# Kernel tuning notes

Hardware: AMD Instinct MI355X
Metric: run time of the kernel (lower is better)

Reference implementation:

```python
import jax, jax.numpy as jnp
import numpy as np

B, T, LATENT, FFN, TEMB = 4, 4096, 256, 1024, 2048
D = 8 * LATENT  # 2048
LN_EPS = 1e-5


def setup_inputs() -> dict:
    key = jax.random.key(0)
    ks = jax.random.split(key, 12)
    s1 = 1.0 / np.sqrt(LATENT)
    s2 = 1.0 / np.sqrt(FFN)
    sd = 1.0 / np.sqrt(D)
    st = 1.0 / np.sqrt(TEMB)
    return {
        "x": jax.random.normal(ks[0], (B, T, D), dtype=jnp.float32),
        "emb": jax.random.normal(ks[1], (B, TEMB), dtype=jnp.float32),
        # 8 parallel branch weights, batched along leading expert axis
        "W1": jax.random.uniform(ks[2], (8, LATENT, FFN), jnp.float32, -s1, s1),
        "b1": jax.random.uniform(ks[3], (8, FFN), jnp.float32, -s1, s1),
        "W2": jax.random.uniform(ks[4], (8, FFN, LATENT), jnp.float32, -s2, s2),
        "b2": jax.random.uniform(ks[5], (8, LATENT), jnp.float32, -s2, s2),
        # StylizationBlock params (latent_dim*8 = D)
        "emb_W": jax.random.uniform(ks[6], (TEMB, 2 * D), jnp.float32, -st, st),
        "emb_b": jax.random.uniform(ks[7], (2 * D,), jnp.float32, -st, st),
        "ln_g": jnp.ones((D,), jnp.float32),
        "ln_b": jnp.zeros((D,), jnp.float32),
        "out_W": jax.random.uniform(ks[8], (D, D), jnp.float32, -sd, sd),
        "out_b": jax.random.uniform(ks[9], (D,), jnp.float32, -sd, sd),
    }


def _layernorm(h, g, b):
    mu = jnp.mean(h, axis=-1, keepdims=True)
    var = jnp.mean(jnp.square(h - mu), axis=-1, keepdims=True)
    return (h - mu) * jax.lax.rsqrt(var + LN_EPS) * g + b


def reference(x, emb, W1, b1, W2, b2, emb_W, emb_b, ln_g, ln_b, out_W, out_b):
    Bx, Tx, Dx = x.shape
    xr = x.reshape(Bx, Tx, 8, LATENT)  # (B,T,8,latent)
    # 8 parallel Linear->GELU->Linear chains as batched GEMMs
    h = jnp.einsum("btel,elf->btef", xr, W1) + b1  # (B,T,8,ffn)
    h = jax.nn.gelu(h, approximate=False)  # dropout=0 (eval)
    y = jnp.einsum("btef,efl->btel", h, W2) + b2  # (B,T,8,latent)
    y = y.reshape(Bx, Tx, Dx)  # concat along channels
    # StylizationBlock: scale/shift from time emb, LN, SiLU, Linear
    eo = jax.nn.silu(emb) @ emb_W + emb_b  # (B, 2D)
    scale, shift = jnp.split(eo[:, None, :], 2, axis=-1)  # (B,1,D) each
    hn = _layernorm(y, ln_g, ln_b) * (1.0 + scale) + shift
    proj = jax.nn.silu(hn) @ out_W + out_b  # (B,T,D)
    return x + proj
```

## Files before the change

### kernel.cpp

```cpp
#include <hip/hip_runtime.h>

typedef __attribute__((ext_vector_type(8))) __bf16 bf16x8;
typedef __attribute__((ext_vector_type(4))) __bf16 bf16x4;
typedef __attribute__((ext_vector_type(4))) float f32x4;

#define TOKENS 16384
#define DDIM   2048
#define LAT    256
#define FFND   1024

__global__ void transpose_f32_bf16(const float* __restrict__ src, __bf16* __restrict__ dst,
                                   int R, int C) {
  __shared__ float tile[32][33];
  const int b = blockIdx.z;
  src += (size_t)b * R * C;
  dst += (size_t)b * R * C;
  const int c0 = blockIdx.x * 32, r0 = blockIdx.y * 32;
  const int tx = threadIdx.x & 31, ty = threadIdx.x >> 5;
  for (int i = ty; i < 32; i += 8)
    tile[i][tx] = src[(size_t)(r0 + i) * C + c0 + tx];
  __syncthreads();
  for (int i = ty; i < 32; i += 8)
    dst[(size_t)(c0 + i) * R + r0 + tx] = (__bf16)tile[tx][i];
}

__global__ void k0_partial(const float* __restrict__ emb, const float* __restrict__ embW,
                           float* __restrict__ pp) {
  __shared__ float se[4 * 256];
  const int tid = threadIdx.x;
  const int kc = blockIdx.y;
  const int kb = kc * 256;
  for (int i = tid; i < 1024; i += 256) {
    const int bb = i >> 8, kk = i & 255;
    float v = emb[bb * 2048 + kb + kk];
    se[i] = v / (1.f + __expf(-v));
  }
  __syncthreads();
  const int j = blockIdx.x * 256 + tid;
  float a0 = 0.f, a1 = 0.f, a2 = 0.f, a3 = 0.f;
  for (int k = 0; k < 256; ++k) {
    float wv = embW[(size_t)(kb + k) * 4096 + j];
    a0 += se[k] * wv;
    a1 += se[256 + k] * wv;
    a2 += se[512 + k] * wv;
    a3 += se[768 + k] * wv;
  }
  pp[(size_t)(kc * 4 + 0) * 4096 + j] = a0;
  pp[(size_t)(kc * 4 + 1) * 4096 + j] = a1;
  pp[(size_t)(kc * 4 + 2) * 4096 + j] = a2;
  pp[(size_t)(kc * 4 + 3) * 4096 + j] = a3;
}

__global__ void k0_reduce(const float* __restrict__ pp, const float* __restrict__ embb,
                          float* __restrict__ ss) {
  const int j = blockIdx.x * 256 + threadIdx.x;
  const float bb = embb[j];
#pragma unroll
  for (int b = 0; b < 4; ++b) {
    float s = bb;
#pragma unroll
    for (int kc = 0; kc < 8; ++kc) s += pp[(size_t)(kc * 4 + b) * 4096 + j];
    ss[b * 4096 + j] = s;
  }
}

__launch_bounds__(256, 2)
__global__ void k1_expert_ffn(const float* __restrict__ x, const __bf16* __restrict__ W1T,
                              const float* __restrict__ b1, const __bf16* __restrict__ W2T,
                              const float* __restrict__ b2, __bf16* __restrict__ y) {
  __shared__ __bf16 xs[64 * 256];
  __shared__ __bf16 hs[64 * 256];

  const int tid = threadIdx.x;
  const int w = tid >> 6;
  const int lane = tid & 63;
  const int q = lane >> 4;
  const int ln = lane & 15;
  const int m0 = blockIdx.x * 64;
  const int e = blockIdx.y;

  {
    const int r0 = tid >> 6;
    const int c = (tid & 63) * 4;
#pragma unroll
    for (int p = 0; p < 16; ++p) {
      const int r = r0 + p * 4;
      f32x4 v = *(const f32x4*)(x + (size_t)(m0 + r) * DDIM + e * LAT + c);
      bf16x4 o;
      o[0] = (__bf16)v[0]; o[1] = (__bf16)v[1]; o[2] = (__bf16)v[2]; o[3] = (__bf16)v[3];
      *(bf16x4*)(xs + r * 256 + c) = o;
    }
  }

  f32x4 acc_y[4][4];
#pragma unroll
  for (int j = 0; j < 4; ++j) {
    float bv = b2[e * LAT + w * 64 + j * 16 + ln];
    f32x4 t = {bv, bv, bv, bv};
#pragma unroll
    for (int i = 0; i < 4; ++i) acc_y[i][j] = t;
  }

  __syncthreads();

  for (int fc = 0; fc < 4; ++fc) {
    f32x4 acc_h[4][4];
#pragma unroll
    for (int j = 0; j < 4; ++j) {
      float bv = b1[e * FFND + fc * 256 + w * 64 + j * 16 + ln];
      f32x4 t = {bv, bv, bv, bv};
#pragma unroll
      for (int i = 0; i < 4; ++i) acc_h[i][j] = t;
    }

    const __bf16* w1src = W1T + ((size_t)e * FFND + fc * 256 + w * 64) * LAT;
    for (int k0 = 0; k0 < 256; k0 += 32) {
      bf16x8 af[4], bfr[4];
#pragma unroll
      for (int j = 0; j < 4; ++j)
        bfr[j] = *(const bf16x8*)(w1src + (size_t)(j * 16 + ln) * LAT + k0 + q * 8);
#pragma unroll
      for (int i = 0; i < 4; ++i)
        af[i] = *(const bf16x8*)(xs + (i * 16 + ln) * 256 + k0 + q * 8);
#pragma unroll
      for (int i = 0; i < 4; ++i)
#pragma unroll
        for (int j = 0; j < 4; ++j)
          acc_h[i][j] = __builtin_amdgcn_mfma_f32_16x16x32_bf16(af[i], bfr[j], acc_h[i][j], 0, 0, 0);
    }

    __syncthreads();

#pragma unroll
    for (int i = 0; i < 4; ++i)
#pragma unroll
      for (int j = 0; j < 4; ++j) {
        const int fl = w * 64 + j * 16 + ln;
#pragma unroll
        for (int r = 0; r < 4; ++r) {
          float vv = acc_h[i][j][r];
          float ge = 0.5f * vv * (1.0f + erff(vv * 0.70710678118654752f));
          hs[(i * 16 + q * 4 + r) * 256 + fl] = (__bf16)ge;
        }
      }

    __syncthreads();

    const __bf16* w2src = W2T + ((size_t)e * LAT + w * 64) * FFND + fc * 256;
    for (int k0 = 0; k0 < 256; k0 += 32) {
      bf16x8 af[4], bfr[4];
#pragma unroll
      for (int j = 0; j < 4; ++j)
        bfr[j] = *(const bf16x8*)(w2src + (size_t)(j * 16 + ln) * FFND + k0 + q * 8);
#pragma unroll
      for (int i = 0; i < 4; ++i)
        af[i] = *(const bf16x8*)(hs + (i * 16 + ln) * 256 + k0 + q * 8);
#pragma unroll
      for (int i = 0; i < 4; ++i)
#pragma unroll
        for (int j = 0; j < 4; ++j)
          acc_y[i][j] = __builtin_amdgcn_mfma_f32_16x16x32_bf16(af[i], bfr[j], acc_y[i][j], 0, 0, 0);
    }
  }

#pragma unroll
  for (int i = 0; i < 4; ++i)
#pragma unroll
    for (int j = 0; j < 4; ++j) {
      const int l = w * 64 + j * 16 + ln;
#pragma unroll
      for (int r = 0; r < 4; ++r) {
        const int m = i * 16 + q * 4 + r;
        y[(size_t)(m0 + m) * DDIM + e * LAT + l] = (__bf16)acc_y[i][j][r];
      }
    }
}

__global__ void k2_ln_mod_silu(const float* __restrict__ ss, const float* __restrict__ g,
                               const float* __restrict__ bb, __bf16* __restrict__ y) {
  __shared__ float red[8];
  const int t = blockIdx.x;
  const int b = t >> 12;
  const int tid = threadIdx.x;
  __bf16* row = y + (size_t)t * DDIM;
  bf16x8 v8 = *(bf16x8*)(row + tid * 8);
  float v[8], s = 0.f, sq = 0.f;
#pragma unroll
  for (int i = 0; i < 8; ++i) {
    v[i] = (float)v8[i];
    s += v[i];
    sq += v[i] * v[i];
  }
#pragma unroll
  for (int off = 32; off > 0; off >>= 1) {
    s += __shfl_down(s, off);
    sq += __shfl_down(sq, off);
  }
  if ((tid & 63) == 0) {
    red[tid >> 6] = s;
    red[4 + (tid >> 6)] = sq;
  }
  __syncthreads();
  const float S = red[0] + red[1] + red[2] + red[3];
  const float SQ = red[4] + red[5] + red[6] + red[7];
  const float mean = S * (1.f / DDIM);
  const float var = SQ * (1.f / DDIM) - mean * mean;
  const float rstd = rsqrtf(var + 1e-5f);
  const float* sc = ss + (size_t)b * 2 * DDIM;
#pragma unroll
  for (int i = 0; i < 8; ++i) {
    const int d = tid * 8 + i;
    float hn = (v[i] - mean) * rstd * g[d] + bb[d];
    hn = hn * (1.f + sc[d]) + sc[DDIM + d];
    float si = hn / (1.f + __expf(-hn));
    v8[i] = (__bf16)si;
  }
  *(bf16x8*)(row + tid * 8) = v8;
}

__launch_bounds__(256, 2)
__global__ void k3_proj(const __bf16* __restrict__ a, const __bf16* __restrict__ oWT,
                        const float* __restrict__ ob, const float* __restrict__ x,
                        float* __restrict__ out, int m_base) {
  __shared__ __bf16 As[128 * 64];
  __shared__ __bf16 Bs[128 * 64];
  const int tid = threadIdx.x;
  const int w = tid >> 6, lane = tid & 63, q = lane >> 4, ln = lane & 15;
  const int wm = w >> 1, wn = w & 1;
  const int m0 = m_base + blockIdx.x * 128, n0 = blockIdx.y * 128;
  f32x4 acc[4][4] = {};
  const int r0 = tid >> 3, c = (tid & 7) * 8;

  for (int k0 = 0; k0 < 2048; k0 += 64) {
    __syncthreads();
#pragma unroll
    for (int p = 0; p < 4; ++p) {
      const int r = r0 + p * 32;
      *(bf16x8*)(As + r * 64 + c) =
          *(const bf16x8*)(a + (size_t)(m0 + r) * DDIM + k0 + c);
      *(bf16x8*)(Bs + r * 64 + c) =
          *(const bf16x8*)(oWT + (size_t)(n0 + r) * DDIM + k0 + c);
    }
    __syncthreads();
#pragma unroll
    for (int ks = 0; ks < 64; ks += 32) {
      bf16x8 af[4], bfr[4];
#pragma unroll
      for (int i = 0; i < 4; ++i)
        af[i] = *(const bf16x8*)(As + (wm * 64 + i * 16 + ln) * 64 + ks + q * 8);
#pragma unroll
      for (int j = 0; j < 4; ++j)
        bfr[j] = *(const bf16x8*)(Bs + (wn * 64 + j * 16 + ln) * 64 + ks + q * 8);
#pragma unroll
      for (int i = 0; i < 4; ++i)
#pragma unroll
        for (int j = 0; j < 4; ++j)
          acc[i][j] = __builtin_amdgcn_mfma_f32_16x16x32_bf16(af[i], bfr[j], acc[i][j], 0, 0, 0);
    }
  }

#pragma unroll
  for (int j = 0; j < 4; ++j) {
    const int n = n0 + wn * 64 + j * 16 + ln;
    const float bn = ob[n];
#pragma unroll
    for (int i = 0; i < 4; ++i)
#pragma unroll
      for (int r = 0; r < 4; ++r) {
        const int m = m0 + wm * 64 + i * 16 + q * 4 + r;
        float v = acc[i][j][r] + bn + x[(size_t)m * DDIM + n];
        out[(size_t)m * DDIM + n] = v;
      }
  }
}

extern "C" void kernel_launch(void* const* d_in, const int* in_sizes, int n_in,
                              void* d_out, int out_size, void* d_ws, size_t ws_size,
                              hipStream_t stream) {
  const float* x    = (const float*)d_in[0];
  const float* emb  = (const float*)d_in[1];
  const float* W1   = (const float*)d_in[2];
  const float* b1   = (const float*)d_in[3];
  const float* W2   = (const float*)d_in[4];
  const float* b2   = (const float*)d_in[5];
  const float* embW = (const float*)d_in[6];
  const float* embb = (const float*)d_in[7];
  const float* lng  = (const float*)d_in[8];
  const float* lnb  = (const float*)d_in[9];
  const float* outW = (const float*)d_in[10];
  const float* outb = (const float*)d_in[11];
  float* out = (float*)d_out;

  char* ob = (char*)d_out;
  __bf16* W1T  = (__bf16*)ob;
  __bf16* W2T  = (__bf16*)(ob + (4 << 20));
  float*  pp   = (float*)(ob + (8 << 20));
  float*  ss   = (float*)(ob + (8 << 20) + (512 << 10));
  __bf16* oWT1 = (__bf16*)ob;
  __bf16* y    = (__bf16*)d_ws;
  __bf16* oWT2 = (__bf16*)((char*)d_ws + (8 << 20));

  transpose_f32_bf16<<<dim3(32, 8, 8), 256, 0, stream>>>(W1, W1T, 256, 1024);
  transpose_f32_bf16<<<dim3(8, 32, 8), 256, 0, stream>>>(W2, W2T, 1024, 256);
  k0_partial<<<dim3(16, 8), 256, 0, stream>>>(emb, embW, pp);
  k0_reduce<<<16, 256, 0, stream>>>(pp, embb, ss);
  k1_expert_ffn<<<dim3(TOKENS / 64, 8), 256, 0, stream>>>(x, W1T, b1, W2T, b2, y);
  k2_ln_mod_silu<<<TOKENS, 256, 0, stream>>>(ss, lng, lnb, y);
  transpose_f32_bf16<<<dim3(64, 64, 1), 256, 0, stream>>>(outW, oWT1, 2048, 2048);
  k3_proj<<<dim3(112, 16), 256, 0, stream>>>(y, oWT1, outb, x, out, 2048);
  transpose_f32_bf16<<<dim3(64, 64, 1), 256, 0, stream>>>(outW, oWT2, 2048, 2048);
  k3_proj<<<dim3(16, 16), 256, 0, stream>>>(y, oWT2, outb, x, out, 0);
}
```

Measured before the change: 903.0 us.

## Swizzle LDS tiles and swap MFMA operands for vectorized epilogue stores

Applies an XOR swizzle to the shared-memory tiles in the expert FFN and projection kernels to avoid LDS bank conflicts on the bf16x8 fragment reads. The MFMA operands are swapped so each lane holds 4 contiguous output columns, which turns scalar scattered epilogue stores (GELU hidden tile, y output, final residual add) into vector bf16x4/f32x4 stores and loads. The k loops are also fully unrolled. The cost is higher register pressure from the unrolling under launch_bounds(256,2), and the swizzle has to match exactly between writers and readers.

```diff
diff --git a/kernel.cpp b/kernel.cpp
--- a/kernel.cpp
+++ b/kernel.cpp
@@ -78,6 +78,7 @@
   const int ln = lane & 15;
   const int m0 = blockIdx.x * 64;
   const int e = blockIdx.y;
+  const int swz = (ln & 7) << 3;
 
   {
     const int r0 = tid >> 6;
@@ -88,17 +89,16 @@
       f32x4 v = *(const f32x4*)(x + (size_t)(m0 + r) * DDIM + e * LAT + c);
       bf16x4 o;
       o[0] = (__bf16)v[0]; o[1] = (__bf16)v[1]; o[2] = (__bf16)v[2]; o[3] = (__bf16)v[3];
-      *(bf16x4*)(xs + r * 256 + c) = o;
+      *(bf16x4*)(xs + r * 256 + (c ^ ((r & 7) << 3))) = o;
     }
   }
 
   f32x4 acc_y[4][4];
 #pragma unroll
   for (int j = 0; j < 4; ++j) {
-    float bv = b2[e * LAT + w * 64 + j * 16 + ln];
-    f32x4 t = {bv, bv, bv, bv};
-#pragma unroll
-    for (int i = 0; i < 4; ++i) acc_y[i][j] = t;
+    f32x4 bv = *(const f32x4*)(b2 + e * LAT + w * 64 + j * 16 + q * 4);
+#pragma unroll
+    for (int i = 0; i < 4; ++i) acc_y[j][i] = bv;
   }
 
   __syncthreads();
@@ -107,13 +107,13 @@
     f32x4 acc_h[4][4];
 #pragma unroll
     for (int j = 0; j < 4; ++j) {
-      float bv = b1[e * FFND + fc * 256 + w * 64 + j * 16 + ln];
-      f32x4 t = {bv, bv, bv, bv};
-#pragma unroll
-      for (int i = 0; i < 4; ++i) acc_h[i][j] = t;
+      f32x4 bv = *(const f32x4*)(b1 + e * FFND + fc * 256 + w * 64 + j * 16 + q * 4);
+#pragma unroll
+      for (int i = 0; i < 4; ++i) acc_h[j][i] = bv;
     }
 
     const __bf16* w1src = W1T + ((size_t)e * FFND + fc * 256 + w * 64) * LAT;
+#pragma unroll
     for (int k0 = 0; k0 < 256; k0 += 32) {
       bf16x8 af[4], bfr[4];
 #pragma unroll
@@ -121,32 +121,36 @@
         bfr[j] = *(const bf16x8*)(w1src + (size_t)(j * 16 + ln) * LAT + k0 + q * 8);
 #pragma unroll
       for (int i = 0; i < 4; ++i)
-        af[i] = *(const bf16x8*)(xs + (i * 16 + ln) * 256 + k0 + q * 8);
-#pragma unroll
-      for (int i = 0; i < 4; ++i)
-#pragma unroll
-        for (int j = 0; j < 4; ++j)
-          acc_h[i][j] = __builtin_amdgcn_mfma_f32_16x16x32_bf16(af[i], bfr[j], acc_h[i][j], 0, 0, 0);
+        af[i] = *(const bf16x8*)(xs + (i * 16 + ln) * 256 + ((k0 + q * 8) ^ swz));
+#pragma unroll
+      for (int j = 0; j < 4; ++j)
+#pragma unroll
+        for (int i = 0; i < 4; ++i)
+          acc_h[j][i] = __builtin_amdgcn_mfma_f32_16x16x32_bf16(bfr[j], af[i], acc_h[j][i], 0, 0, 0);
     }
 
     __syncthreads();
 
 #pragma unroll
-    for (int i = 0; i < 4; ++i)
-#pragma unroll
-      for (int j = 0; j < 4; ++j) {
-        const int fl = w * 64 + j * 16 + ln;
+    for (int j = 0; j < 4; ++j)
+#pragma unroll
+      for (int i = 0; i < 4; ++i) {
+        const int tok = i * 16 + ln;
+        const int fcol = w * 64 + j * 16 + q * 4;
+        bf16x4 o;
 #pragma unroll
         for (int r = 0; r < 4; ++r) {
-          float vv = acc_h[i][j][r];
+          float vv = acc_h[j][i][r];
           float ge = 0.5f * vv * (1.0f + erff(vv * 0.70710678118654752f));
-          hs[(i * 16 + q * 4 + r) * 256 + fl] = (__bf16)ge;
+          o[r] = (__bf16)ge;
         }
+        *(bf16x4*)(hs + tok * 256 + (fcol ^ swz)) = o;
       }
 
     __syncthreads();
 
     const __bf16* w2src = W2T + ((size_t)e * LAT + w * 64) * FFND + fc * 256;
+#pragma unroll
     for (int k0 = 0; k0 < 256; k0 += 32) {
       bf16x8 af[4], bfr[4];
 #pragma unroll
@@ -154,25 +158,25 @@
         bfr[j] = *(const bf16x8*)(w2src + (size_t)(j * 16 + ln) * FFND + k0 + q * 8);
 #pragma unroll
       for (int i = 0; i < 4; ++i)
-        af[i] = *(const bf16x8*)(hs + (i * 16 + ln) * 256 + k0 + q * 8);
-#pragma unroll
-      for (int i = 0; i < 4; ++i)
-#pragma unroll
-        for (int j = 0; j < 4; ++j)
-          acc_y[i][j] = __builtin_amdgcn_mfma_f32_16x16x32_bf16(af[i], bfr[j], acc_y[i][j], 0, 0, 0);
-    }
-  }
-
-#pragma unroll
-  for (int i = 0; i < 4; ++i)
-#pragma unroll
-    for (int j = 0; j < 4; ++j) {
-      const int l = w * 64 + j * 16 + ln;
-#pragma unroll
-      for (int r = 0; r < 4; ++r) {
-        const int m = i * 16 + q * 4 + r;
-        y[(size_t)(m0 + m) * DDIM + e * LAT + l] = (__bf16)acc_y[i][j][r];
-      }
+        af[i] = *(const bf16x8*)(hs + (i * 16 + ln) * 256 + ((k0 + q * 8) ^ swz));
+#pragma unroll
+      for (int j = 0; j < 4; ++j)
+#pragma unroll
+        for (int i = 0; i < 4; ++i)
+          acc_y[j][i] = __builtin_amdgcn_mfma_f32_16x16x32_bf16(bfr[j], af[i], acc_y[j][i], 0, 0, 0);
+    }
+  }
+
+#pragma unroll
+  for (int j = 0; j < 4; ++j)
+#pragma unroll
+    for (int i = 0; i < 4; ++i) {
+      const int tok = i * 16 + ln;
+      const int l = w * 64 + j * 16 + q * 4;
+      bf16x4 o;
+#pragma unroll
+      for (int r = 0; r < 4; ++r) o[r] = (__bf16)acc_y[j][i][r];
+      *(bf16x4*)(y + (size_t)(m0 + tok) * DDIM + e * LAT + l) = o;
     }
 }
 
@@ -228,6 +232,7 @@
   const int w = tid >> 6, lane = tid & 63, q = lane >> 4, ln = lane & 15;
   const int wm = w >> 1, wn = w & 1;
   const int m0 = m_base + blockIdx.x * 128, n0 = blockIdx.y * 128;
+  const int swz = (ln & 7) << 3;
   f32x4 acc[4][4] = {};
   const int r0 = tid >> 3, c = (tid & 7) * 8;
 
@@ -236,9 +241,10 @@
 #pragma unroll
     for (int p = 0; p < 4; ++p) {
       const int r = r0 + p * 32;
-      *(bf16x8*)(As + r * 64 + c) =
+      const int cs = c ^ ((r & 7) << 3);
+      *(bf16x8*)(As + r * 64 + cs) =
           *(const bf16x8*)(a + (size_t)(m0 + r) * DDIM + k0 + c);
-      *(bf16x8*)(Bs + r * 64 + c) =
+      *(bf16x8*)(Bs + r * 64 + cs) =
           *(const bf16x8*)(oWT + (size_t)(n0 + r) * DDIM + k0 + c);
     }
     __syncthreads();
@@ -247,30 +253,31 @@
       bf16x8 af[4], bfr[4];
 #pragma unroll
       for (int i = 0; i < 4; ++i)
-        af[i] = *(const bf16x8*)(As + (wm * 64 + i * 16 + ln) * 64 + ks + q * 8);
-#pragma unroll
-      for (int j = 0; j < 4; ++j)
-        bfr[j] = *(const bf16x8*)(Bs + (wn * 64 + j * 16 + ln) * 64 + ks + q * 8);
-#pragma unroll
-      for (int i = 0; i < 4; ++i)
-#pragma unroll
-        for (int j = 0; j < 4; ++j)
-          acc[i][j] = __builtin_amdgcn_mfma_f32_16x16x32_bf16(af[i], bfr[j], acc[i][j], 0, 0, 0);
+        af[i] = *(const bf16x8*)(As + (wm * 64 + i * 16 + ln) * 64 + ((ks + q * 8) ^ swz));
+#pragma unroll
+      for (int j = 0; j < 4; ++j)
+        bfr[j] = *(const bf16x8*)(Bs + (wn * 64 + j * 16 + ln) * 64 + ((ks + q * 8) ^ swz));
+#pragma unroll
+      for (int j = 0; j < 4; ++j)
+#pragma unroll
+        for (int i = 0; i < 4; ++i)
+          acc[j][i] = __builtin_amdgcn_mfma_f32_16x16x32_bf16(bfr[j], af[i], acc[j][i], 0, 0, 0);
     }
   }
 
 #pragma unroll
   for (int j = 0; j < 4; ++j) {
-    const int n = n0 + wn * 64 + j * 16 + ln;
-    const float bn = ob[n];
-#pragma unroll
-    for (int i = 0; i < 4; ++i)
-#pragma unroll
-      for (int r = 0; r < 4; ++r) {
-        const int m = m0 + wm * 64 + i * 16 + q * 4 + r;
-        float v = acc[i][j][r] + bn + x[(size_t)m * DDIM + n];
-        out[(size_t)m * DDIM + n] = v;
-      }
+    const int n = n0 + wn * 64 + j * 16 + q * 4;
+    const f32x4 bn4 = *(const f32x4*)(ob + n);
+#pragma unroll
+    for (int i = 0; i < 4; ++i) {
+      const int m = m0 + wm * 64 + i * 16 + ln;
+      const f32x4 xr = *(const f32x4*)(x + (size_t)m * DDIM + n);
+      f32x4 v;
+#pragma unroll
+      for (int r = 0; r < 4; ++r) v[r] = acc[j][i][r] + bn4[r] + xr[r];
+      *(f32x4*)(out + (size_t)m * DDIM + n) = v;
+    }
   }
 }
 
```

Result: faster. 865.5 us (-4.1%).
